# Kernel optimization log

Measured on AMD Instinct MI355X. Metric: run time of the kernel, lower is better.

Reference implementation:

```python
import jax, jax.numpy as jnp
import numpy as np

BS, D_IN, D_H, D_Z = 4096, 784, 400, 20


def setup_inputs() -> dict:
    key = jax.random.key(0)
    ks = jax.random.split(key, 13)
    s = 0.05
    return {
        "x": jax.random.normal(ks[0], (BS, D_IN), dtype=jnp.float32),
        "W1": jax.random.normal(ks[1], (D_H, D_IN), dtype=jnp.float32) * s,
        "b1": jax.random.normal(ks[2], (D_H,), dtype=jnp.float32) * s,
        "W21": jax.random.normal(ks[3], (D_Z, D_H), dtype=jnp.float32) * s,
        "b21": jax.random.normal(ks[4], (D_Z,), dtype=jnp.float32) * s,
        "W22": jax.random.normal(ks[5], (D_Z, D_H), dtype=jnp.float32) * s,
        "b22": jax.random.normal(ks[6], (D_Z,), dtype=jnp.float32) * s,
        "W3": jax.random.normal(ks[7], (D_H, D_Z), dtype=jnp.float32) * s,
        "b3": jax.random.normal(ks[8], (D_H,), dtype=jnp.float32) * s,
        "W41": jax.random.normal(ks[9], (D_IN, D_H), dtype=jnp.float32) * s,
        "b41": jax.random.normal(ks[10], (D_IN,), dtype=jnp.float32) * s,
        "W42": jax.random.normal(ks[11], (D_IN, D_H), dtype=jnp.float32) * s,
        "b42": jax.random.normal(ks[12], (D_IN,), dtype=jnp.float32) * s,
    }


def reference(x, W1, b1, W21, b21, W22, b22, W3, b3, W41, b41, W42, b42):
    xr = x.reshape(-1, D_IN)                              # [bs, 784]
    # encode
    h1 = jax.nn.relu(xr @ W1.T + b1)                      # [bs, 400]
    mu = h1 @ W21.T + b21                                 # [bs, 20]
    logvar = h1 @ W22.T + b22                             # [bs, 20]
    # unscented sigma points: varsqrt[:, i] = sqrt(N)*logvar[:, i]*e_i
    N = D_Z
    sqrtN = jnp.asarray(np.sqrt(N), dtype=x.dtype)
    # delta[i, b, j] = sqrt(N) * logvar[b, i] * (i == j)   -> [N, bs, N]
    delta = sqrtN * logvar.T[:, :, None] * jnp.eye(N, dtype=x.dtype)[:, None, :]
    z = jnp.concatenate([mu[None] + delta, mu[None] - delta], axis=0)  # [2N, bs, N]

    def decode(zs):
        h3 = jax.nn.relu(zs @ W3.T + b3)                  # [bs, 400]
        return zs @ W41.T * 0 + (h3 @ W41.T + b41), h3 @ W42.T + b42

    def decode_clean(zs):
        h3 = jax.nn.relu(zs @ W3.T + b3)
        return h3 @ W41.T + b41, h3 @ W42.T + b42

    # original loop decodes every sigma point; recon_x keeps the last one
    mu_x, var_x = jax.vmap(decode_clean)(z)               # each [2N, bs, 784]
    recon_mu = mu_x[-1]
    recon_var = var_x[-1]
    return recon_mu, recon_var, mu, logvar, z
```

## Files before the change

### kernel.cpp

```cpp
#include <hip/hip_runtime.h>
#include <hip/hip_bf16.h>

#define BS   4096
#define DIN  784
#define DH   400
#define DZ   20

#define KP1  832
#define KPH  416
#define KPD  448

#define OFF_RMU  0
#define OFF_RVAR 3211264
#define OFF_MU   6422528
#define OFF_LV   6504448
#define OFF_Z    6586368

#define WS_WCAT  0
#define WS_W2C   1404928
#define WS_W1B   1444864
#define WS_H1B   2110464
#define WS_H3B   5518336

#define SQRT20F 4.47213595499958f

using short8 = __attribute__((ext_vector_type(8))) short;
using f4     = __attribute__((ext_vector_type(4))) float;
using i4     = __attribute__((ext_vector_type(4))) int;

__device__ __forceinline__ short bf16r(float f) {
    union { float f; unsigned u; } v; v.f = f;
    unsigned r = (v.u + 0x7fffu + ((v.u >> 16) & 1u)) >> 16;
    return (short)r;
}

__device__ __forceinline__ i4 pack8(const i4 q0, const i4 q1) {
    i4 d;
    d[0] = (q0[1] & 0xffff0000) | (int)(((unsigned)q0[0]) >> 16);
    d[1] = (q0[3] & 0xffff0000) | (int)(((unsigned)q0[2]) >> 16);
    d[2] = (q1[1] & 0xffff0000) | (int)(((unsigned)q1[0]) >> 16);
    d[3] = (q1[3] & 0xffff0000) | (int)(((unsigned)q1[2]) >> 16);
    return d;
}

__device__ __forceinline__ void glds16(const void* g, void* l) {
    __builtin_amdgcn_global_load_lds(
        (const __attribute__((address_space(1))) unsigned int*)g,
        (__attribute__((address_space(3))) unsigned int*)l,
        16, 0, 0);
}

__global__ void k0(const float* __restrict__ W1, const float* __restrict__ W41,
                   const float* __restrict__ W42, const float* __restrict__ W21,
                   const float* __restrict__ W22, char* __restrict__ ws) {
    const int N0 = 400 * 104;
    const int N1 = N0 + 1568 * 56;
    const int N2 = N1 + 48 * 52;
    int gid = blockIdx.x * 256 + threadIdx.x;
    if (gid >= N2) return;

    const float* sr = nullptr;
    short* dst;
    int c, DC;
    if (gid < N0) {
        int row = gid / 104; c = gid - row * 104; DC = 98;
        sr = W1 + (size_t)row * DIN;
        dst = (short*)(ws + WS_W1B) + (size_t)row * KP1 + c * 8;
    } else if (gid < N1) {
        int p = gid - N0;
        int row = p / 56; c = p - row * 56; DC = 50;
        sr = (row < 784) ? (W41 + (size_t)row * DH) : (W42 + (size_t)(row - 784) * DH);
        dst = (short*)(ws + WS_WCAT) + (size_t)row * KPD + c * 8;
    } else {
        int p = gid - N1;
        int row = p / 52; c = p - row * 52; DC = 50;
        if (row < 20)      sr = W21 + (size_t)row * DH;
        else if (row < 40) sr = W22 + (size_t)(row - 20) * DH;
        else               sr = nullptr;
        dst = (short*)(ws + WS_W2C) + (size_t)row * KPH + c * 8;
    }
    short8 v;
    if (c < DC && sr) {
        f4 a = *(const f4*)(sr + c * 8);
        f4 b = *(const f4*)(sr + c * 8 + 4);
#pragma unroll
        for (int e = 0; e < 4; ++e) { v[e] = bf16r(a[e]); v[4 + e] = bf16r(b[e]); }
    } else {
#pragma unroll
        for (int e = 0; e < 8; ++e) v[e] = 0;
    }
    *(short8*)dst = v;
}

__global__ __launch_bounds__(256)
void k1(const float* __restrict__ x, const float* __restrict__ b1,
        const short* __restrict__ W1b, short* __restrict__ h1b) {
    __shared__ short sA[2][64 * 64];
    __shared__ short sB[2][80 * 64];

    const int tid = threadIdx.x;
    const int bid = blockIdx.x;
    const int swz = (bid & 7) * 40 + (bid >> 3);
    const int bm = swz / 5, bn = swz - bm * 5;
    const int w = tid >> 6, l = tid & 63, lg = l >> 4, lr = l & 15;

    f4 acc[5] = {};
    i4 ar[4];

    auto a_load = [&](int kt) {
#pragma unroll
        for (int i = 0; i < 2; ++i) {
            int c = tid + i * 256;
            int row = c >> 3, kc = c & 7;
            int gk = kt * 64 + kc * 8;
            if (gk < DIN) {
                const i4* p = (const i4*)(x + (size_t)(bm * 64 + row) * DIN + gk);
                ar[2 * i] = p[0]; ar[2 * i + 1] = p[1];
            } else {
                ar[2 * i] = (i4){0, 0, 0, 0};
                ar[2 * i + 1] = (i4){0, 0, 0, 0};
            }
        }
    };
    auto a_write = [&](int buf) {
#pragma unroll
        for (int i = 0; i < 2; ++i) {
            int c = tid + i * 256;
            int row = c >> 3, kc = c & 7;
            *(i4*)&sA[buf][(row * 8 + (kc ^ (row & 7))) * 8] = pack8(ar[2 * i], ar[2 * i + 1]);
        }
    };
    auto b_stage = [&](int buf, int kt) {
#pragma unroll
        for (int it = 0; it < 3; ++it) {
            int p = it * 256 + tid;
            if (p < 640) {
                int r = p >> 3, kc = (p & 7) ^ (r & 7);
                glds16(W1b + (size_t)(bn * 80 + r) * KP1 + kt * 64 + kc * 8, &sB[buf][p * 8]);
            }
        }
    };
    auto compute = [&](int buf) {
        const int row = w * 16 + lr;
#pragma unroll
        for (int kk = 0; kk < 2; ++kk) {
            short8 a = *(const short8*)&sA[buf][(row * 8 + ((kk * 4 + lg) ^ (row & 7))) * 8];
#pragma unroll
            for (int ni = 0; ni < 5; ++ni) {
                int brw = ni * 16 + lr;
                short8 b = *(const short8*)&sB[buf][(brw * 8 + ((kk * 4 + lg) ^ (brw & 7))) * 8];
                acc[ni] = __builtin_amdgcn_mfma_f32_16x16x32_bf16(a, b, acc[ni], 0, 0, 0);
            }
        }
    };

    a_load(0); b_stage(0, 0); a_write(0);
    __syncthreads();
    for (int kt = 0; kt < 13; ++kt) {
        const int cur = kt & 1;
        if (kt < 12) { a_load(kt + 1); b_stage(cur ^ 1, kt + 1); }
        compute(cur);
        if (kt < 12) a_write(cur ^ 1);
        __syncthreads();
    }

#pragma unroll
    for (int ni = 0; ni < 5; ++ni) {
        int col = bn * 80 + ni * 16 + lr;
        float bias = b1[col];
#pragma unroll
        for (int r = 0; r < 4; ++r) {
            int row = bm * 64 + w * 16 + lg * 4 + r;
            float v = acc[ni][r] + bias;
            h1b[(size_t)row * KPH + col] = bf16r(v > 0.f ? v : 0.f);
        }
    }
    if (bn == 4) {
        for (int p = tid; p < 64 * 16; p += 256) {
            int r = p >> 4, c = 400 + (p & 15);
            h1b[(size_t)(bm * 64 + r) * KPH + c] = 0;
        }
    }
}

__global__ __launch_bounds__(512, 1)
void k_mid(const short* __restrict__ h1b, const short* __restrict__ w2c,
           const float* __restrict__ W3, const float* __restrict__ b3,
           const float* __restrict__ b21, const float* __restrict__ b22,
           float* __restrict__ out, short* __restrict__ h3b) {
    __shared__ short sA[16 * 416];
    __shared__ short sB[48 * 416];
    __shared__ short sW[400 * 40];
    __shared__ float muv[2][16][20];
    __shared__ short zl[16 * 40];
    __shared__ short h3s[16 * 448];

    const int tid = threadIdx.x;
    const int blk = blockIdx.x;
    const int w = tid >> 6, l = tid & 63, lg = l >> 4, lr = l & 15;
    const int r0 = blk * 16;

#pragma unroll
    for (int it = 0; it < 2; ++it) {
        int p = it * 512 + tid;
        if (p < 832) {
            int r = p / 52, cp = p - r * 52, c = cp ^ (r & 3);
            glds16(h1b + (size_t)(r0 + r) * KPH + c * 8, &sA[p * 8]);
        }
    }
#pragma unroll
    for (int it = 0; it < 5; ++it) {
        int p = it * 512 + tid;
        if (p < 2496) {
            int r = p / 52, cp = p - r * 52, c = cp ^ (r & 3);
            glds16(w2c + (size_t)r * KPH + c * 8, &sB[p * 8]);
        }
    }
    if (tid < 400) {
        int r = tid;
        const float* src = W3 + (size_t)r * DZ;
        f4 f0 = *(const f4*)src;
        f4 f1 = *(const f4*)(src + 4);
        f4 f2 = *(const f4*)(src + 8);
        f4 f3 = *(const f4*)(src + 12);
        f4 f5 = *(const f4*)(src + 16);
        short8 c0, c1, c2, c3;
#pragma unroll
        for (int e = 0; e < 4; ++e) {
            c0[e] = bf16r(f0[e]); c0[4 + e] = bf16r(f1[e]);
            c1[e] = bf16r(f2[e]); c1[4 + e] = bf16r(f3[e]);
            c2[e] = bf16r(f5[e]); c2[4 + e] = 0;
            c3[e] = 0; c3[4 + e] = 0;
        }
        *(short8*)&sW[r * 40 + 0]  = c0;
        *(short8*)&sW[r * 40 + 8]  = c1;
        *(short8*)&sW[r * 40 + 16] = c2;
        *(short8*)&sW[r * 40 + 24] = c3;
    }
    __syncthreads();

    if (w == 0) {
        f4 a3[3] = {};
#pragma unroll
        for (int kk = 0; kk < 13; ++kk) {
            short8 a = *(const short8*)&sA[(lr * 52 + ((kk * 4 + lg) ^ (lr & 3))) * 8];
#pragma unroll
            for (int ni = 0; ni < 3; ++ni) {
                int br = ni * 16 + lr;
                short8 b = *(const short8*)&sB[(br * 52 + ((kk * 4 + lg) ^ (br & 3))) * 8];
                a3[ni] = __builtin_amdgcn_mfma_f32_16x16x32_bf16(a, b, a3[ni], 0, 0, 0);
            }
        }
#pragma unroll
        for (int ni = 0; ni < 3; ++ni) {
            int n = ni * 16 + lr;
            if (n < 40) {
                float bias = (n < 20) ? b21[n] : b22[n - 20];
#pragma unroll
                for (int r = 0; r < 4; ++r) {
                    int row = lg * 4 + r;
                    float v = a3[ni][r] + bias;
                    if (n < 20) {
                        muv[0][row][n] = v;
                        out[OFF_MU + (size_t)(r0 + row) * 20 + n] = v;
                    } else {
                        muv[1][row][n - 20] = v;
                        out[OFF_LV + (size_t)(r0 + row) * 20 + (n - 20)] = v;
                    }
                }
            }
        }
    }
    __syncthreads();

    if (tid < 80) {
        int row = tid / 5, c = tid - (tid / 5) * 5;
        short8 v;
#pragma unroll
        for (int e = 0; e < 8; ++e) {
            int j = c * 8 + e;
            float val = 0.f;
            if (j < 20) {
                val = muv[0][row][j];
                if (j == 19) val -= SQRT20F * muv[1][row][19];
            }
            v[e] = bf16r(val);
        }
        *(short8*)&zl[row * 40 + c * 8] = v;
    } else if (tid < 176) {
        int t = tid - 80;
        int row = t / 6, c = t - (t / 6) * 6;
        short8 zz;
#pragma unroll
        for (int e = 0; e < 8; ++e) zz[e] = 0;
        *(short8*)&h3s[row * 448 + 400 + c * 8] = zz;
    }
#pragma unroll
    for (int it = 0; it < 7; ++it) {
        int p = it * 512 + tid;
        if (p < 3200) {
            int s = p / 80, q = p - s * 80;
            int row = q / 5, j4 = q - (q / 5) * 5;
            f4 v = *(const f4*)&muv[0][row][j4 * 4];
            int sp = (s < 20) ? s : s - 20;
            if ((sp >> 2) == j4) {
                float add = ((s < 20) ? SQRT20F : -SQRT20F) * muv[1][row][sp];
                int e = sp & 3;
#pragma unroll
                for (int k = 0; k < 4; ++k) v[k] += (e == k) ? add : 0.f;
            }
            *(f4*)(out + OFF_Z + ((size_t)s * BS + r0 + row) * 20 + j4 * 4) = v;
        }
    }
    __syncthreads();

    for (int f = w; f < 25; f += 8) {
        int n0 = f * 16;
        short8 a = *(const short8*)&zl[lr * 40 + lg * 8];
        short8 b = *(const short8*)&sW[(n0 + lr) * 40 + lg * 8];
        f4 z4 = {};
        f4 accv = __builtin_amdgcn_mfma_f32_16x16x32_bf16(a, b, z4, 0, 0, 0);
        int n = n0 + lr;
        float bias = b3[n];
#pragma unroll
        for (int r = 0; r < 4; ++r) {
            int row = lg * 4 + r;
            float v = accv[r] + bias;
            h3s[row * 448 + n] = bf16r(v > 0.f ? v : 0.f);
        }
    }
    __syncthreads();

#pragma unroll
    for (int it = 0; it < 2; ++it) {
        int p = it * 512 + tid;
        if (p < 896) {
            int row = p / 56, c = p - (p / 56) * 56;
            *(short8*)(h3b + (size_t)(r0 + row) * KPD + c * 8) =
                *(const short8*)&h3s[row * 448 + c * 8];
        }
    }
}

__global__ __launch_bounds__(512)
void k_gemm4(const short* __restrict__ h3b, const short* __restrict__ wcat,
             const float* __restrict__ b41, const float* __restrict__ b42,
             float* __restrict__ out) {
    __shared__ short sA[2][128 * 64];
    __shared__ short sB[2][112 * 64];

    const int tid = threadIdx.x;
    const int bid = blockIdx.x;
    const int swz = (bid & 7) * 56 + (bid >> 3);
    const int bm = swz / 14, bn = swz - bm * 14;
    const int w = tid >> 6, l = tid & 63, lg = l >> 4, lr = l & 15;

    f4 acc[7] = {};

    auto stage = [&](int buf, int kt) {
#pragma unroll
        for (int i = 0; i < 2; ++i) {
            int c = tid + i * 512;
            int r = c >> 3, kc = (c & 7) ^ (r & 7);
            glds16(h3b + (size_t)(bm * 128 + r) * KPD + kt * 64 + kc * 8, &sA[buf][c * 8]);
        }
#pragma unroll
        for (int i = 0; i < 2; ++i) {
            int c = tid + i * 512;
            if (c < 896) {
                int r = c >> 3, kc = (c & 7) ^ (r & 7);
                glds16(wcat + (size_t)(bn * 112 + r) * KPD + kt * 64 + kc * 8, &sB[buf][c * 8]);
            }
        }
    };

    stage(0, 0);
    __syncthreads();
    for (int kt = 0; kt < 7; ++kt) {
        const int cur = kt & 1;
        if (kt < 6) stage(cur ^ 1, kt + 1);
        const int row = w * 16 + lr;
#pragma unroll
        for (int kk = 0; kk < 2; ++kk) {
            short8 a = *(const short8*)&sA[cur][(row * 8 + ((kk * 4 + lg) ^ (row & 7))) * 8];
#pragma unroll
            for (int ni = 0; ni < 7; ++ni) {
                int br = ni * 16 + lr;
                short8 b = *(const short8*)&sB[cur][(br * 8 + ((kk * 4 + lg) ^ (br & 7))) * 8];
                acc[ni] = __builtin_amdgcn_mfma_f32_16x16x32_bf16(a, b, acc[ni], 0, 0, 0);
            }
        }
        __syncthreads();
    }

    const bool first = (bn < 7);
#pragma unroll
    for (int ni = 0; ni < 7; ++ni) {
        int colt = bn * 112 + ni * 16 + lr;
        int cc = first ? colt : colt - 784;
        float bias = first ? b41[cc] : b42[cc];
        size_t base = first ? (size_t)OFF_RMU : (size_t)OFF_RVAR;
#pragma unroll
        for (int r = 0; r < 4; ++r) {
            size_t row = (size_t)(bm * 128 + w * 16 + lg * 4 + r);
            out[base + row * DIN + cc] = acc[ni][r] + bias;
        }
    }
}

extern "C" void kernel_launch(void* const* d_in, const int* in_sizes, int n_in,
                              void* d_out, int out_size, void* d_ws, size_t ws_size,
                              hipStream_t stream) {
    const float* x   = (const float*)d_in[0];
    const float* W1  = (const float*)d_in[1];
    const float* b1  = (const float*)d_in[2];
    const float* W21 = (const float*)d_in[3];
    const float* b21 = (const float*)d_in[4];
    const float* W22 = (const float*)d_in[5];
    const float* b22 = (const float*)d_in[6];
    const float* W3  = (const float*)d_in[7];
    const float* b3  = (const float*)d_in[8];
    const float* W41 = (const float*)d_in[9];
    const float* b41 = (const float*)d_in[10];
    const float* W42 = (const float*)d_in[11];
    const float* b42 = (const float*)d_in[12];

    float* out = (float*)d_out;
    char*  ws  = (char*)d_ws;
    const short* wcat = (const short*)(ws + WS_WCAT);
    const short* w2c  = (const short*)(ws + WS_W2C);
    const short* W1b  = (const short*)(ws + WS_W1B);
    short* h1b = (short*)(ws + WS_H1B);
    short* h3b = (short*)(ws + WS_H3B);

    k0<<<516, 256, 0, stream>>>(W1, W41, W42, W21, W22, ws);
    k1<<<320, 256, 0, stream>>>(x, b1, W1b, h1b);
    k_mid<<<256, 512, 0, stream>>>(h1b, w2c, W3, b3, b21, b22, out, h3b);
    k_gemm4<<<448, 512, 0, stream>>>(h3b, wcat, b41, b42, out);
}
```

Baseline: 43.37 us.

## Overlap decoder weight conversion with first GEMM and enlarge k1 row tile

Trims the weight conversion kernel to W1 only and moves the W41/W42/W21/W22 bf16 conversion into extra blocks of k1, so that conversion runs alongside the h1 GEMM instead of before it. k1 now uses 512 threads with a 128-row M tile, which halves the number of GEMM blocks and lets each staged W1 tile serve more rows. The conversion blocks take grid slots from the GEMM, and the larger tile raises LDS use and lowers block-level parallelism.

After: 45.43 us. +4.7%, slower.

```diff
diff --git a/kernel.cpp b/kernel.cpp
--- a/kernel.cpp
+++ b/kernel.cpp
@@ -50,39 +50,16 @@
         16, 0, 0);
 }
 
-__global__ void k0(const float* __restrict__ W1, const float* __restrict__ W41,
-                   const float* __restrict__ W42, const float* __restrict__ W21,
-                   const float* __restrict__ W22, char* __restrict__ ws) {
-    const int N0 = 400 * 104;
-    const int N1 = N0 + 1568 * 56;
-    const int N2 = N1 + 48 * 52;
+__global__ void k0(const float* __restrict__ W1, char* __restrict__ ws) {
     int gid = blockIdx.x * 256 + threadIdx.x;
-    if (gid >= N2) return;
-
-    const float* sr = nullptr;
-    short* dst;
-    int c, DC;
-    if (gid < N0) {
-        int row = gid / 104; c = gid - row * 104; DC = 98;
-        sr = W1 + (size_t)row * DIN;
-        dst = (short*)(ws + WS_W1B) + (size_t)row * KP1 + c * 8;
-    } else if (gid < N1) {
-        int p = gid - N0;
-        int row = p / 56; c = p - row * 56; DC = 50;
-        sr = (row < 784) ? (W41 + (size_t)row * DH) : (W42 + (size_t)(row - 784) * DH);
-        dst = (short*)(ws + WS_WCAT) + (size_t)row * KPD + c * 8;
-    } else {
-        int p = gid - N1;
-        int row = p / 52; c = p - row * 52; DC = 50;
-        if (row < 20)      sr = W21 + (size_t)row * DH;
-        else if (row < 40) sr = W22 + (size_t)(row - 20) * DH;
-        else               sr = nullptr;
-        dst = (short*)(ws + WS_W2C) + (size_t)row * KPH + c * 8;
-    }
+    if (gid >= 400 * 104) return;
+    int row = gid / 104, c = gid - row * 104;
+    short* dst = (short*)(ws + WS_W1B) + (size_t)row * KP1 + c * 8;
     short8 v;
-    if (c < DC && sr) {
-        f4 a = *(const f4*)(sr + c * 8);
-        f4 b = *(const f4*)(sr + c * 8 + 4);
+    if (c < 98) {
+        const float* sr = W1 + (size_t)row * DIN + c * 8;
+        f4 a = *(const f4*)sr;
+        f4 b = *(const f4*)(sr + 4);
 #pragma unroll
         for (int e = 0; e < 4; ++e) { v[e] = bf16r(a[e]); v[4 + e] = bf16r(b[e]); }
     } else {
@@ -92,15 +69,55 @@
     *(short8*)dst = v;
 }
 
-__global__ __launch_bounds__(256)
+__global__ __launch_bounds__(512)
 void k1(const float* __restrict__ x, const float* __restrict__ b1,
-        const short* __restrict__ W1b, short* __restrict__ h1b) {
-    __shared__ short sA[2][64 * 64];
+        const short* __restrict__ W1b,
+        const float* __restrict__ W41, const float* __restrict__ W42,
+        const float* __restrict__ W21, const float* __restrict__ W22,
+        short* __restrict__ h1b, char* __restrict__ ws) {
+    __shared__ short sA[2][128 * 64];
     __shared__ short sB[2][80 * 64];
 
     const int tid = threadIdx.x;
     const int bid = blockIdx.x;
-    const int swz = (bid & 7) * 40 + (bid >> 3);
+
+    if (bid >= 160) {
+        short* wcat = (short*)(ws + WS_WCAT);
+        short* w2c  = (short*)(ws + WS_W2C);
+        const int NC = 1568 * 56 + 48 * 52;
+        for (int p = (bid - 160) * 512 + tid; p < NC; p += 64 * 512) {
+            const float* sr = nullptr;
+            short* dst;
+            int c;
+            if (p < 1568 * 56) {
+                int row = p / 56; c = p - row * 56;
+                sr = (row < 784) ? (W41 + (size_t)row * DH)
+                                 : (W42 + (size_t)(row - 784) * DH);
+                dst = wcat + (size_t)row * KPD + c * 8;
+            } else {
+                int q = p - 1568 * 56;
+                int row = q / 52; c = q - row * 52;
+                if (row < 20)      sr = W21 + (size_t)row * DH;
+                else if (row < 40) sr = W22 + (size_t)(row - 20) * DH;
+                else               sr = nullptr;
+                dst = w2c + (size_t)row * KPH + c * 8;
+            }
+            short8 v;
+            if (c < 50 && sr) {
+                f4 a = *(const f4*)(sr + c * 8);
+                f4 b = *(const f4*)(sr + c * 8 + 4);
+#pragma unroll
+                for (int e = 0; e < 4; ++e) { v[e] = bf16r(a[e]); v[4 + e] = bf16r(b[e]); }
+            } else {
+#pragma unroll
+                for (int e = 0; e < 8; ++e) v[e] = 0;
+            }
+            *(short8*)dst = v;
+        }
+        return;
+    }
+
+    const int swz = (bid & 7) * 20 + (bid >> 3);
     const int bm = swz / 5, bn = swz - bm * 5;
     const int w = tid >> 6, l = tid & 63, lg = l >> 4, lr = l & 15;
 
@@ -110,11 +127,11 @@
     auto a_load = [&](int kt) {
 #pragma unroll
         for (int i = 0; i < 2; ++i) {
-            int c = tid + i * 256;
+            int c = tid + i * 512;
             int row = c >> 3, kc = c & 7;
             int gk = kt * 64 + kc * 8;
             if (gk < DIN) {
-                const i4* p = (const i4*)(x + (size_t)(bm * 64 + row) * DIN + gk);
+                const i4* p = (const i4*)(x + (size_t)(bm * 128 + row) * DIN + gk);
                 ar[2 * i] = p[0]; ar[2 * i + 1] = p[1];
             } else {
                 ar[2 * i] = (i4){0, 0, 0, 0};
@@ -125,15 +142,15 @@
     auto a_write = [&](int buf) {
 #pragma unroll
         for (int i = 0; i < 2; ++i) {
-            int c = tid + i * 256;
+            int c = tid + i * 512;
             int row = c >> 3, kc = c & 7;
             *(i4*)&sA[buf][(row * 8 + (kc ^ (row & 7))) * 8] = pack8(ar[2 * i], ar[2 * i + 1]);
         }
     };
     auto b_stage = [&](int buf, int kt) {
 #pragma unroll
-        for (int it = 0; it < 3; ++it) {
-            int p = it * 256 + tid;
+        for (int it = 0; it < 2; ++it) {
+            int p = it * 512 + tid;
             if (p < 640) {
                 int r = p >> 3, kc = (p & 7) ^ (r & 7);
                 glds16(W1b + (size_t)(bn * 80 + r) * KP1 + kt * 64 + kc * 8, &sB[buf][p * 8]);
@@ -170,15 +187,15 @@
         float bias = b1[col];
 #pragma unroll
         for (int r = 0; r < 4; ++r) {
-            int row = bm * 64 + w * 16 + lg * 4 + r;
+            int row = bm * 128 + w * 16 + lg * 4 + r;
             float v = acc[ni][r] + bias;
             h1b[(size_t)row * KPH + col] = bf16r(v > 0.f ? v : 0.f);
         }
     }
     if (bn == 4) {
-        for (int p = tid; p < 64 * 16; p += 256) {
+        for (int p = tid; p < 128 * 16; p += 512) {
             int r = p >> 4, c = 400 + (p & 15);
-            h1b[(size_t)(bm * 64 + r) * KPH + c] = 0;
+            h1b[(size_t)(bm * 128 + r) * KPH + c] = 0;
         }
     }
 }
@@ -433,8 +450,8 @@
     short* h1b = (short*)(ws + WS_H1B);
     short* h3b = (short*)(ws + WS_H3B);
 
-    k0<<<516, 256, 0, stream>>>(W1, W41, W42, W21, W22, ws);
-    k1<<<320, 256, 0, stream>>>(x, b1, W1b, h1b);
+    k0<<<163, 256, 0, stream>>>(W1, ws);
+    k1<<<224, 512, 0, stream>>>(x, b1, W1b, W41, W42, W21, W22, h1b, ws);
     k_mid<<<256, 512, 0, stream>>>(h1b, w2c, W3, b3, b21, b22, out, h3b);
     k_gemm4<<<448, 512, 0, stream>>>(h3b, wcat, b41, b42, out);
 }
```
